# Kernel tuning notes

Measured on AMD Instinct MI355X. Metric: run time of the kernel, lower is better.

The kernel has to match this reference:

```python
import jax, jax.numpy as jnp
import numpy as np

B, A, M, K = 8, 49104, 50, 80  # batch, anchors, max GT boxes, classes
BETA = 1.0 / 9.0               # smooth-L1 transition point
VAR = jnp.array([0.1, 0.1, 0.2, 0.2], dtype=jnp.float32)


def calc_iou(a, b):
    # a: (A,4) anchors, b: (M,4) boxes -> (A,M) IoU
    area_b = (b[:, 2] - b[:, 0]) * (b[:, 3] - b[:, 1])
    area_a = (a[:, 2] - a[:, 0]) * (a[:, 3] - a[:, 1])
    iw = jnp.maximum(jnp.minimum(a[:, 2:3], b[None, :, 2]) - jnp.maximum(a[:, 0:1], b[None, :, 0]), 0.0)
    ih = jnp.maximum(jnp.minimum(a[:, 3:4], b[None, :, 3]) - jnp.maximum(a[:, 1:2], b[None, :, 1]), 0.0)
    inter = iw * ih
    ua = jnp.maximum(area_a[:, None] + area_b[None, :] - inter, 1e-8)
    return inter / ua


def _per_image(logits, reg, bxs, cls, anchors):
    # logits: (A,K) probabilities, reg: (A,4), bxs: (M,4) (-1 padded), cls: (M,) int
    valid = bxs[:, 0] != -1.0                      # (M,)
    iou = calc_iou(anchors, bxs)                   # (A,M)
    iou = jnp.where(valid[None, :], iou, -1.0)     # mask padded boxes
    iou_max = iou.max(axis=1)                      # (A,)
    max_ind = iou.argmax(axis=1)                   # (A,)
    neg = iou_max < 0.4
    pos = iou_max >= 0.5
    a_cls = cls[max_ind]                           # (A,)
    a_box = bxs[max_ind]                           # (A,4)
    # targets: -1 ignore, 0 background, one-hot(class-1) for positives
    onehot = jax.nn.one_hot(a_cls - 1, K, dtype=logits.dtype)
    targets = jnp.where(pos[:, None], onehot, jnp.where(neg[:, None], 0.0, -1.0))
    num_pos = jnp.maximum(pos.sum().astype(logits.dtype), 1.0)
    # focal loss (logits are probabilities)
    p = jnp.clip(logits, 1e-4, 1.0 - 1e-4)
    is_pos_t = targets == 1.0
    alpha = jnp.where(is_pos_t, 0.25, 0.75)
    fw = jnp.where(is_pos_t, 1.0 - p, p)
    bce = -(targets * jnp.log(p) + (1.0 - targets) * jnp.log1p(-p))
    cls_loss = jnp.where(targets != -1.0, alpha * fw * fw * bce, 0.0).sum() / num_pos
    aw = anchors[:, 2] - anchors[:, 0]
    ah = anchors[:, 3] - anchors[:, 1]
    acx = anchors[:, 0] + 0.5 * aw
    acy = anchors[:, 1] + 0.5 * ah
    gw0 = a_box[:, 2] - a_box[:, 0]
    gh0 = a_box[:, 3] - a_box[:, 1]
    gcx = a_box[:, 0] + 0.5 * gw0
    gcy = a_box[:, 1] + 0.5 * gh0
    gw = jnp.maximum(gw0, 1.0)
    gh = jnp.maximum(gh0, 1.0)
    t = jnp.stack([(gcx - acx) / aw, (gcy - acy) / ah, jnp.log(gw / aw), jnp.log(gh / ah)], axis=1) / VAR
    diff = jnp.abs(t - reg)
    sl1 = jnp.where(diff <= BETA, 0.5 * diff * diff / BETA, diff - 0.5 * BETA)
    npos = pos.sum().astype(logits.dtype)
    reg_loss = jnp.where(pos[:, None], sl1, 0.0).sum() / (4.0 * jnp.maximum(npos, 1.0))
    return cls_loss, reg_loss


def reference(cls_logits, reg_preds, anchors, boxes, classes):
    cl, rl = jax.vmap(_per_image, in_axes=(0, 0, 0, 0, None))(cls_logits, reg_preds, boxes, classes, anchors)
    cls_loss = cl.mean()
    reg_loss = rl.mean()
    return cls_loss, reg_loss, cls_loss + reg_loss


def setup_inputs() -> dict:
    key = jax.random.key(0)
    k = jax.random.split(key, 6)
    cls_logits = jax.random.uniform(k[0], (B, A, K), minval=0.02, maxval=0.98, dtype=jnp.float32)
    reg_preds = jax.random.normal(k[1], (B, A, 4), dtype=jnp.float32) * 0.1
    axy = jax.random.uniform(k[2], (A, 2), minval=0.0, maxval=448.0)
    awh = jax.random.uniform(k[3], (A, 2), minval=8.0, maxval=64.0)
    anchors = jnp.concatenate([axy, axy + awh], axis=1)
    bxy = jax.random.uniform(k[4], (B, M, 2), minval=0.0, maxval=384.0)
    bwh = jax.random.uniform(k[5], (B, M, 2), minval=16.0, maxval=128.0)
    boxes = jnp.concatenate([bxy, bxy + bwh], axis=-1)
    nvalid = jax.random.randint(jax.random.fold_in(key, 1), (B,), 1, M + 1)
    vmask = jnp.arange(M)[None, :] < nvalid[:, None]
    boxes = jnp.where(vmask[..., None], boxes, -1.0)
    classes = jax.random.randint(jax.random.fold_in(key, 2), (B, M), 1, K + 1)
    return {"cls_logits": cls_logits, "reg_preds": reg_preds, "anchors": anchors, "boxes": boxes, "classes": classes}
```

## Files before the change

kernel.cpp:

```cpp
#include <hip/hip_runtime.h>
#include <math.h>

#define B_N 8
#define A_N 49104
#define M_N 50
#define K_N 80
#define BETA_C (1.0f / 9.0f)

#define APB   192
#define NBLK  256
#define F4PA  20
#define ITER2 15

typedef float vf4 __attribute__((ext_vector_type(4)));

__device__ __forceinline__ float wred(float v) {
#pragma unroll
    for (int off = 32; off > 0; off >>= 1) v += __shfl_down(v, off, 64);
    return v;
}

__global__ __launch_bounds__(256, 8) void fused_kernel(
    const float* __restrict__ logits,
    const float* __restrict__ reg,
    const float* __restrict__ anchors,
    const float* __restrict__ boxes,
    const int* __restrict__ classes,
    float* __restrict__ clspart,
    float* __restrict__ regpart,
    float* __restrict__ npospart)
{
    const int b   = blockIdx.y;
    const int a0  = blockIdx.x * APB;
    const int tid = threadIdx.x;

    __shared__ float sb[M_N * 4];
    __shared__ int   sc[M_N];
    __shared__ int   sstat[APB];
    if (tid < M_N * 4) sb[tid] = boxes[b * M_N * 4 + tid];
    if (tid < M_N)     sc[tid] = classes[b * M_N + tid];
    __syncthreads();

    float regl = 0.0f;
    float posf = 0.0f;

    if (tid < APB) {
        int s = -1;
        const int a = a0 + tid;
        if (a < A_N) {
            const float4 an = ((const float4*)anchors)[a];
            const float aw = an.z - an.x;
            const float ah = an.w - an.y;
            const float areaA = aw * ah;

            float best = -2.0f;
            int bi = 0;
#pragma unroll 5
            for (int m = 0; m < M_N; ++m) {
                const float bx0 = sb[4 * m + 0];
                const float by0 = sb[4 * m + 1];
                const float bx1 = sb[4 * m + 2];
                const float by1 = sb[4 * m + 3];
                float val = -1.0f;
                if (bx0 != -1.0f) {
                    const float iw = fmaxf(fminf(an.z, bx1) - fmaxf(an.x, bx0), 0.0f);
                    const float ih = fmaxf(fminf(an.w, by1) - fmaxf(an.y, by0), 0.0f);
                    const float inter = iw * ih;
                    const float ua = fmaxf(areaA + (bx1 - bx0) * (by1 - by0) - inter, 1e-8f);
                    val = inter / ua;
                }
                if (val > best) { best = val; bi = m; }
            }

            if (best >= 0.5f) {
                s = sc[bi];
                posf = 1.0f;
                const float4 r = ((const float4*)reg)[b * A_N + a];
                const float gx0 = sb[4 * bi + 0], gy0 = sb[4 * bi + 1];
                const float gx1 = sb[4 * bi + 2], gy1 = sb[4 * bi + 3];
                const float acx = an.x + 0.5f * aw;
                const float acy = an.y + 0.5f * ah;
                const float gw0 = gx1 - gx0;
                const float gh0 = gy1 - gy0;
                const float gcx = gx0 + 0.5f * gw0;
                const float gcy = gy0 + 0.5f * gh0;
                const float gw = fmaxf(gw0, 1.0f);
                const float gh = fmaxf(gh0, 1.0f);
                const float t0 = ((gcx - acx) / aw) / 0.1f;
                const float t1 = ((gcy - acy) / ah) / 0.1f;
                const float t2 = logf(gw / aw) / 0.2f;
                const float t3 = logf(gh / ah) / 0.2f;
                float d, sl;
                d = fabsf(t0 - r.x); sl  = (d <= BETA_C) ? 0.5f * d * d / BETA_C : d - 0.5f * BETA_C;
                d = fabsf(t1 - r.y); sl += (d <= BETA_C) ? 0.5f * d * d / BETA_C : d - 0.5f * BETA_C;
                d = fabsf(t2 - r.z); sl += (d <= BETA_C) ? 0.5f * d * d / BETA_C : d - 0.5f * BETA_C;
                d = fabsf(t3 - r.w); sl += (d <= BETA_C) ? 0.5f * d * d / BETA_C : d - 0.5f * BETA_C;
                regl = sl;
            } else if (best < 0.4f) {
                s = 0;
            }
        }
        sstat[tid] = s;
    }
    __syncthreads();

    const vf4* img4 = (const vf4*)(logits + (size_t)b * ((size_t)A_N * K_N));
    float cls = 0.0f;
#pragma unroll 5
    for (int it = 0; it < ITER2; ++it) {
        const int li = it * 256 + tid;
        const int la = li / F4PA;
        const int fc = li - la * F4PA;
        const int st = sstat[la];
        const int ga = min(a0 + la, A_N - 1);
        const vf4 p4 = __builtin_nontemporal_load(img4 + ((size_t)ga * F4PA + fc));
#pragma unroll
        for (int j = 0; j < 4; ++j) {
            const float p = fminf(fmaxf(p4[j], 1e-4f), 1.0f - 1e-4f);
            const bool ispos = (st >= 1) && (fc * 4 + j == st - 1);
            const float larg = ispos ? p : (1.0f - p);
            const float fw   = 1.0f - larg;
            const float aw   = (st < 0) ? 0.0f : (ispos ? 0.25f : 0.75f);
            cls += aw * fw * fw * (-__logf(larg));
        }
    }

    const float cw = wred(cls);
    const float rw = wred(regl);
    const float pw = wred(posf);
    __shared__ float sred[12];
    const int lane = tid & 63, wid = tid >> 6;
    if (lane == 0) { sred[wid] = cw; sred[4 + wid] = rw; sred[8 + wid] = pw; }
    __syncthreads();
    if (tid == 0) {
        clspart[b * NBLK + blockIdx.x]  = sred[0] + sred[1] + sred[2] + sred[3];
        regpart[b * NBLK + blockIdx.x]  = sred[4] + sred[5] + sred[6] + sred[7];
        npospart[b * NBLK + blockIdx.x] = sred[8] + sred[9] + sred[10] + sred[11];
    }
}

__global__ __launch_bounds__(256) void finalize_kernel(
    const float* __restrict__ clspart,
    const float* __restrict__ regpart,
    const float* __restrict__ npospart,
    float* __restrict__ out)
{
    __shared__ float sred[12];
    float clsAcc = 0.0f, regAcc = 0.0f;

    for (int b = 0; b < B_N; ++b) {
        float cs = 0.0f, rs = 0.0f, np = 0.0f;
        for (int i = threadIdx.x; i < NBLK; i += 256) {
            cs += clspart[b * NBLK + i];
            rs += regpart[b * NBLK + i];
            np += npospart[b * NBLK + i];
        }
        cs = wred(cs); rs = wred(rs); np = wred(np);
        const int lane = threadIdx.x & 63, wid = threadIdx.x >> 6;
        __syncthreads();
        if (lane == 0) { sred[wid] = cs; sred[4 + wid] = rs; sred[8 + wid] = np; }
        __syncthreads();
        if (threadIdx.x == 0) {
            const float csT = sred[0] + sred[1] + sred[2] + sred[3];
            const float rsT = sred[4] + sred[5] + sred[6] + sred[7];
            const float npT = sred[8] + sred[9] + sred[10] + sred[11];
            const float fnp = fmaxf(npT, 1.0f);
            clsAcc += csT / fnp;
            regAcc += rsT / (4.0f * fnp);
        }
    }
    if (threadIdx.x == 0) {
        const float cl = clsAcc / (float)B_N;
        const float rl = regAcc / (float)B_N;
        out[0] = cl;
        out[1] = rl;
        out[2] = cl + rl;
    }
}

extern "C" void kernel_launch(void* const* d_in, const int* in_sizes, int n_in,
                              void* d_out, int out_size, void* d_ws, size_t ws_size,
                              hipStream_t stream) {
    const float* cls_logits = (const float*)d_in[0];
    const float* reg_preds  = (const float*)d_in[1];
    const float* anchors    = (const float*)d_in[2];
    const float* boxes      = (const float*)d_in[3];
    const int*   classes    = (const int*)d_in[4];
    float* out = (float*)d_out;

    char* ws = (char*)d_ws;
    float* clspart  = (float*)ws; ws += (size_t)B_N * NBLK * sizeof(float);
    float* regpart  = (float*)ws; ws += (size_t)B_N * NBLK * sizeof(float);
    float* npospart = (float*)ws;

    dim3 g1(NBLK, B_N);
    fused_kernel<<<g1, 256, 0, stream>>>(cls_logits, reg_preds, anchors, boxes,
                                         classes, clspart, regpart, npospart);
    finalize_kernel<<<1, 256, 0, stream>>>(clspart, regpart, npospart, out);
}
```

Measured before the change: 211.4 us.

## Prefetch logits before IoU matching and simplify focal-loss math

Issues the first five vector loads of each block's logits tile into registers before the IoU/argmax phase, so memory latency overlaps the matching compute. The focal loss is rewritten to apply the negative-class term uniformly with log2 and folded constants, plus a per-vector correction only for the one positive class element, which removes per-element select logic. The finalize kernel is parallelised across batches with 32-lane reductions instead of a serial per-batch loop. Occupancy hint drops from 8 to 6 waves to make room for the prefetch registers, at the cost of fewer resident blocks.

```diff
diff --git a/kernel.cpp b/kernel.cpp
--- a/kernel.cpp
+++ b/kernel.cpp
@@ -11,6 +11,10 @@
 #define NBLK  256
 #define F4PA  20
 #define ITER2 15
+#define PF    5
+
+#define C_NEG 0.51986039f
+#define C_POS 0.17328680f
 
 typedef float vf4 __attribute__((ext_vector_type(4)));
 
@@ -20,7 +24,7 @@
     return v;
 }
 
-__global__ __launch_bounds__(256, 8) void fused_kernel(
+__global__ __launch_bounds__(256, 6) void fused_kernel(
     const float* __restrict__ logits,
     const float* __restrict__ reg,
     const float* __restrict__ anchors,
@@ -33,40 +37,50 @@
     const int b   = blockIdx.y;
     const int a0  = blockIdx.x * APB;
     const int tid = threadIdx.x;
-
-    __shared__ float sb[M_N * 4];
-    __shared__ int   sc[M_N];
-    __shared__ int   sstat[APB];
-    if (tid < M_N * 4) sb[tid] = boxes[b * M_N * 4 + tid];
-    if (tid < M_N)     sc[tid] = classes[b * M_N + tid];
-    __syncthreads();
+    const int a   = a0 + tid;
+
+    __shared__ float4 sb4[M_N];
+    __shared__ int    sc[M_N];
+    __shared__ int    sstat[APB];
+
+    if (tid < M_N) {
+        sb4[tid] = ((const float4*)boxes)[b * M_N + tid];
+        sc[tid]  = classes[b * M_N + tid];
+    }
+    const float4 an = ((const float4*)anchors)[min(a, A_N - 1)];
+    __syncthreads();
+
+    const vf4* img4 = (const vf4*)(logits + (size_t)b * ((size_t)A_N * K_N));
+    vf4 pf[PF];
+#pragma unroll
+    for (int it = 0; it < PF; ++it) {
+        const int li = it * 256 + tid;
+        const int la = li / F4PA;
+        const int fc = li - la * F4PA;
+        const int ga = min(a0 + la, A_N - 1);
+        pf[it] = __builtin_nontemporal_load(img4 + ((size_t)ga * F4PA + fc));
+    }
 
     float regl = 0.0f;
     float posf = 0.0f;
-
     if (tid < APB) {
         int s = -1;
-        const int a = a0 + tid;
         if (a < A_N) {
-            const float4 an = ((const float4*)anchors)[a];
             const float aw = an.z - an.x;
             const float ah = an.w - an.y;
             const float areaA = aw * ah;
 
             float best = -2.0f;
             int bi = 0;
-#pragma unroll 5
+#pragma unroll 2
             for (int m = 0; m < M_N; ++m) {
-                const float bx0 = sb[4 * m + 0];
-                const float by0 = sb[4 * m + 1];
-                const float bx1 = sb[4 * m + 2];
-                const float by1 = sb[4 * m + 3];
+                const float4 bb = sb4[m];
                 float val = -1.0f;
-                if (bx0 != -1.0f) {
-                    const float iw = fmaxf(fminf(an.z, bx1) - fmaxf(an.x, bx0), 0.0f);
-                    const float ih = fmaxf(fminf(an.w, by1) - fmaxf(an.y, by0), 0.0f);
+                if (bb.x != -1.0f) {
+                    const float iw = fmaxf(fminf(an.z, bb.z) - fmaxf(an.x, bb.x), 0.0f);
+                    const float ih = fmaxf(fminf(an.w, bb.w) - fmaxf(an.y, bb.y), 0.0f);
                     const float inter = iw * ih;
-                    const float ua = fmaxf(areaA + (bx1 - bx0) * (by1 - by0) - inter, 1e-8f);
+                    const float ua = fmaxf(areaA + (bb.z - bb.x) * (bb.w - bb.y) - inter, 1e-8f);
                     val = inter / ua;
                 }
                 if (val > best) { best = val; bi = m; }
@@ -76,14 +90,13 @@
                 s = sc[bi];
                 posf = 1.0f;
                 const float4 r = ((const float4*)reg)[b * A_N + a];
-                const float gx0 = sb[4 * bi + 0], gy0 = sb[4 * bi + 1];
-                const float gx1 = sb[4 * bi + 2], gy1 = sb[4 * bi + 3];
+                const float4 g = sb4[bi];
                 const float acx = an.x + 0.5f * aw;
                 const float acy = an.y + 0.5f * ah;
-                const float gw0 = gx1 - gx0;
-                const float gh0 = gy1 - gy0;
-                const float gcx = gx0 + 0.5f * gw0;
-                const float gcy = gy0 + 0.5f * gh0;
+                const float gw0 = g.z - g.x;
+                const float gh0 = g.w - g.y;
+                const float gcx = g.x + 0.5f * gw0;
+                const float gcy = g.y + 0.5f * gh0;
                 const float gw = fmaxf(gw0, 1.0f);
                 const float gh = fmaxf(gh0, 1.0f);
                 const float t0 = ((gcx - acx) / aw) / 0.1f;
@@ -104,26 +117,49 @@
     }
     __syncthreads();
 
-    const vf4* img4 = (const vf4*)(logits + (size_t)b * ((size_t)A_N * K_N));
     float cls = 0.0f;
-#pragma unroll 5
-    for (int it = 0; it < ITER2; ++it) {
+#define PROC(P4)                                                               \
+    {                                                                          \
+        const int st = sstat[la];             \
+        const float wgt = (st < 0) ? 0.0f : -C_NEG;                            \
+        _Pragma("unroll")                                                      \
+        for (int j = 0; j < 4; ++j) {                                          \
+            const float p  = fminf(fmaxf((P4)[j], 1e-4f), 1.0f - 1e-4f);       \
+            const float om = 1.0f - p;                                         \
+            const float t  = (p * p) * __log2f(om);                 \
+            cls = fmaf(wgt, t, cls);                                           \
+        }                                                                      \
+        if (st >= 1) {                             \
+            const unsigned jo = (unsigned)(st - 1 - 4 * fc);                   \
+            if (jo < 4u) {                 \
+                const float pj = (jo == 0) ? (P4)[0] : (jo == 1) ? (P4)[1]     \
+                               : (jo == 2) ? (P4)[2] : (P4)[3];                \
+                const float pc = fminf(fmaxf(pj, 1e-4f), 1.0f - 1e-4f);        \
+                const float om = 1.0f - pc;                                    \
+                const float t  = (pc * pc) * __log2f(om);                      \
+                cls = fmaf(C_NEG, t, cls);                  \
+                cls = fmaf((C_POS * om) * om, -__log2f(pc), cls);     \
+            }                                                                  \
+        }                                                                      \
+    }
+
+#pragma unroll
+    for (int it = 0; it < PF; ++it) {
         const int li = it * 256 + tid;
         const int la = li / F4PA;
         const int fc = li - la * F4PA;
-        const int st = sstat[la];
+        PROC(pf[it]);
+    }
+#pragma unroll 5
+    for (int it = PF; it < ITER2; ++it) {
+        const int li = it * 256 + tid;
+        const int la = li / F4PA;
+        const int fc = li - la * F4PA;
         const int ga = min(a0 + la, A_N - 1);
         const vf4 p4 = __builtin_nontemporal_load(img4 + ((size_t)ga * F4PA + fc));
-#pragma unroll
-        for (int j = 0; j < 4; ++j) {
-            const float p = fminf(fmaxf(p4[j], 1e-4f), 1.0f - 1e-4f);
-            const bool ispos = (st >= 1) && (fc * 4 + j == st - 1);
-            const float larg = ispos ? p : (1.0f - p);
-            const float fw   = 1.0f - larg;
-            const float aw   = (st < 0) ? 0.0f : (ispos ? 0.25f : 0.75f);
-            cls += aw * fw * fw * (-__logf(larg));
-        }
-    }
+        PROC(p4);
+    }
+#undef PROC
 
     const float cw = wred(cls);
     const float rw = wred(regl);
@@ -145,31 +181,34 @@
     const float* __restrict__ npospart,
     float* __restrict__ out)
 {
-    __shared__ float sred[12];
-    float clsAcc = 0.0f, regAcc = 0.0f;
-
-    for (int b = 0; b < B_N; ++b) {
-        float cs = 0.0f, rs = 0.0f, np = 0.0f;
-        for (int i = threadIdx.x; i < NBLK; i += 256) {
-            cs += clspart[b * NBLK + i];
-            rs += regpart[b * NBLK + i];
-            np += npospart[b * NBLK + i];
+    const int tid = threadIdx.x;
+    const int bb  = tid >> 5;
+    const int l5  = tid & 31;
+    float cs = 0.0f, rs = 0.0f, np = 0.0f;
+#pragma unroll
+    for (int i = 0; i < NBLK / 32; ++i) {
+        const int idx = bb * NBLK + l5 + i * 32;
+        cs += clspart[idx];
+        rs += regpart[idx];
+        np += npospart[idx];
+    }
+#pragma unroll
+    for (int off = 16; off > 0; off >>= 1) {
+        cs += __shfl_down(cs, off, 32);
+        rs += __shfl_down(rs, off, 32);
+        np += __shfl_down(np, off, 32);
+    }
+    __shared__ float scs[B_N], srs[B_N], snp[B_N];
+    if (l5 == 0) { scs[bb] = cs; srs[bb] = rs; snp[bb] = np; }
+    __syncthreads();
+    if (tid == 0) {
+        float clsAcc = 0.0f, regAcc = 0.0f;
+#pragma unroll
+        for (int i = 0; i < B_N; ++i) {
+            const float fnp = fmaxf(snp[i], 1.0f);
+            clsAcc += scs[i] / fnp;
+            regAcc += srs[i] / (4.0f * fnp);
         }
-        cs = wred(cs); rs = wred(rs); np = wred(np);
-        const int lane = threadIdx.x & 63, wid = threadIdx.x >> 6;
-        __syncthreads();
-        if (lane == 0) { sred[wid] = cs; sred[4 + wid] = rs; sred[8 + wid] = np; }
-        __syncthreads();
-        if (threadIdx.x == 0) {
-            const float csT = sred[0] + sred[1] + sred[2] + sred[3];
-            const float rsT = sred[4] + sred[5] + sred[6] + sred[7];
-            const float npT = sred[8] + sred[9] + sred[10] + sred[11];
-            const float fnp = fmaxf(npT, 1.0f);
-            clsAcc += csT / fnp;
-            regAcc += rsT / (4.0f * fnp);
-        }
-    }
-    if (threadIdx.x == 0) {
         const float cl = clsAcc / (float)B_N;
         const float rl = regAcc / (float)B_N;
         out[0] = cl;
```

Result: faster. 189.5 us (-10.4%).
